# Kernel optimization log

Measured on AMD Instinct MI355X. Metric: run time of the kernel, lower is better.

The kernel has to match this reference:

```python
import jax, jax.numpy as jnp
import numpy as np

N_NODES = 50000

def _gcn_conv(x, W, b, src, dst, norm, n_nodes):
    # PyG GCNConv: linear transform, then normalized scatter-add aggregation.
    h = x @ W                                   # [N, out]
    msg = h[src] * norm[:, None]                # [E', out] gather + scale
    out = jax.ops.segment_sum(msg, dst, num_segments=n_nodes)  # scatter-add
    return out + b

def _norm_edges(edge_index, n_nodes):
    # Add self loops, compute symmetric deg^{-1/2} normalization (PyG default).
    loops = jnp.arange(n_nodes, dtype=edge_index.dtype)
    src = jnp.concatenate([edge_index[0], loops])
    dst = jnp.concatenate([edge_index[1], loops])
    deg = jax.ops.segment_sum(jnp.ones_like(dst, dtype=jnp.float32), dst,
                              num_segments=n_nodes)
    dinv = jnp.where(deg > 0, jax.lax.rsqrt(deg), 0.0)
    norm = dinv[src] * dinv[dst]
    return src, dst, norm

def setup_inputs() -> dict:
    key = jax.random.key(0)
    k1, k2, k3, k4, k5 = jax.random.split(key, 5)
    d_in, d_hid, d_out = 128, 96, 64
    x = jax.random.normal(k1, (N_NODES, d_in), dtype=jnp.float32)
    edge_index = jax.random.randint(k2, (2, 800000), 0, N_NODES, dtype=jnp.int32)
    W1 = jax.random.normal(k3, (d_in, d_hid), dtype=jnp.float32) / np.sqrt(d_in)
    b1 = jnp.zeros((d_hid,), dtype=jnp.float32)
    W2 = jax.random.normal(k4, (d_hid, d_out), dtype=jnp.float32) / np.sqrt(d_hid)
    b2 = jnp.zeros((d_out,), dtype=jnp.float32)
    return {"x": x, "edge_index": edge_index, "W1": W1, "b1": b1, "W2": W2, "b2": b2}

def reference(x, edge_index, W1, b1, W2, b2):
    n = x.shape[0]
    src, dst, norm = _norm_edges(edge_index, n)
    h = jax.nn.relu(_gcn_conv(x, W1, b1, src, dst, norm, n))
    # dropout is identity in eval mode
    out = jax.nn.relu(_gcn_conv(h, W2, b2, src, dst, norm, n))
    return out
```

## Files before the change

### kernel.cpp

```cpp
#include <hip/hip_runtime.h>

#define D_IN 128
#define D_HID 96
#define D_OUT 64
#define CHUNK 4096

template <int K, int C, int BM>
__global__ void gemm1_deg_kernel(const float* __restrict__ X, const float* __restrict__ W,
                                 float* __restrict__ H, int n, int nblkGemm,
                                 const int* __restrict__ dst, int* __restrict__ deg, int E) {
    constexpr int KT = 32;
    constexpr int TX = C / 4;
    constexpr int TY = BM / 4;
    constexpr int NTH = TX * TY;
    constexpr int WS = C + 4;
    constexpr int XS = KT + 4;
    __shared__ float Wl[KT * WS];
    __shared__ float Xl[BM * XS];

    const int tx = threadIdx.x, ty = threadIdx.y;
    const int tlin = ty * TX + tx;

    if (blockIdx.x >= nblkGemm) {
        int e0 = ((blockIdx.x - nblkGemm) * NTH + tlin) * 4;
        if (e0 + 3 < E) {
            int4 d = *(const int4*)&dst[e0];
            atomicAdd(&deg[d.x], 1);
            atomicAdd(&deg[d.y], 1);
            atomicAdd(&deg[d.z], 1);
            atomicAdd(&deg[d.w], 1);
        } else {
            for (int j = 0; j < 4; ++j) {
                int e = e0 + j;
                if (e < E) atomicAdd(&deg[dst[e]], 1);
            }
        }
        return;
    }

    const int r0 = blockIdx.x * BM;
    const int row0 = ty * 4;

    float4 acc0 = {0,0,0,0}, acc1 = {0,0,0,0}, acc2 = {0,0,0,0}, acc3 = {0,0,0,0};

    for (int kt0 = 0; kt0 < K; kt0 += KT) {
        for (int q = tlin; q < KT * (C / 4); q += NTH) {
            int k = q / (C / 4), cq = q % (C / 4);
            *(float4*)&Wl[k * WS + cq * 4] = *(const float4*)&W[(long)(kt0 + k) * C + cq * 4];
        }
        for (int q = tlin; q < BM * (KT / 4); q += NTH) {
            int r = q / (KT / 4), kq = q % (KT / 4);
            int gr = r0 + r; if (gr >= n) gr = n - 1;
            *(float4*)&Xl[r * XS + kq * 4] = *(const float4*)&X[(long)gr * K + kt0 + kq * 4];
        }
        __syncthreads();
#pragma unroll 4
        for (int k = 0; k < KT; ++k) {
            float4 w = *(const float4*)&Wl[k * WS + tx * 4];
            float x0 = Xl[(row0 + 0) * XS + k];
            float x1 = Xl[(row0 + 1) * XS + k];
            float x2 = Xl[(row0 + 2) * XS + k];
            float x3 = Xl[(row0 + 3) * XS + k];
            acc0.x = fmaf(x0, w.x, acc0.x); acc0.y = fmaf(x0, w.y, acc0.y);
            acc0.z = fmaf(x0, w.z, acc0.z); acc0.w = fmaf(x0, w.w, acc0.w);
            acc1.x = fmaf(x1, w.x, acc1.x); acc1.y = fmaf(x1, w.y, acc1.y);
            acc1.z = fmaf(x1, w.z, acc1.z); acc1.w = fmaf(x1, w.w, acc1.w);
            acc2.x = fmaf(x2, w.x, acc2.x); acc2.y = fmaf(x2, w.y, acc2.y);
            acc2.z = fmaf(x2, w.z, acc2.z); acc2.w = fmaf(x2, w.w, acc2.w);
            acc3.x = fmaf(x3, w.x, acc3.x); acc3.y = fmaf(x3, w.y, acc3.y);
            acc3.z = fmaf(x3, w.z, acc3.z); acc3.w = fmaf(x3, w.w, acc3.w);
        }
        __syncthreads();
    }

    float4 a[4] = {acc0, acc1, acc2, acc3};
#pragma unroll
    for (int i = 0; i < 4; ++i) {
        int row = r0 + row0 + i;
        if (row < n) *(float4*)&H[(long)row * C + tx * 4] = a[i];
    }
}

__global__ void scanA_kernel(const int* __restrict__ deg, int* __restrict__ partial, int n) {
    __shared__ int wsum[16];
    const int tid = threadIdx.x, lane = tid & 63, wid = tid >> 6;
    int i0 = blockIdx.x * CHUNK + tid * 4;
    int s = 0;
    if (i0 + 3 < n) {
        int4 v = *(const int4*)&deg[i0];
        s = v.x + v.y + v.z + v.w;
    } else {
        for (int j = 0; j < 4; ++j) if (i0 + j < n) s += deg[i0 + j];
    }
    for (int off = 32; off; off >>= 1) s += __shfl_down(s, off);
    if (lane == 0) wsum[wid] = s;
    __syncthreads();
    if (tid == 0) {
        int t = 0;
        for (int w = 0; w < 16; ++w) t += wsum[w];
        partial[blockIdx.x] = t;
    }
}

__global__ void scanB_kernel(const int* __restrict__ partial, int* __restrict__ offs, int nb) {
    int lane = threadIdx.x;
    int v = (lane < nb) ? partial[lane] : 0;
    int s = v;
    for (int off = 1; off < 64; off <<= 1) {
        int t = __shfl_up(s, off);
        if (lane >= off) s += t;
    }
    if (lane < nb) offs[lane] = s - v;
}

__global__ void scanC_kernel(const int* __restrict__ deg, const int* __restrict__ offs,
                             int* __restrict__ row_ptr, int* __restrict__ cursor,
                             float* __restrict__ dinv, int n) {
    __shared__ int wsum[16];
    const int tid = threadIdx.x, lane = tid & 63, wid = tid >> 6;
    const int base = offs[blockIdx.x];
    int i0 = blockIdx.x * CHUNK + tid * 4;
    int v0 = (i0 + 0 < n) ? deg[i0 + 0] : 0;
    int v1 = (i0 + 1 < n) ? deg[i0 + 1] : 0;
    int v2 = (i0 + 2 < n) ? deg[i0 + 2] : 0;
    int v3 = (i0 + 3 < n) ? deg[i0 + 3] : 0;
    int p0 = v0, p1 = p0 + v1, p2 = p1 + v2, p3 = p2 + v3;
    int tsum = p3;
    for (int off = 1; off < 64; off <<= 1) {
        int t = __shfl_up(tsum, off);
        if (lane >= off) tsum += t;
    }
    if (lane == 63) wsum[wid] = tsum;
    __syncthreads();
    if (wid == 0) {
        int w = (lane < 16) ? wsum[lane] : 0;
        for (int off = 1; off < 16; off <<= 1) {
            int t = __shfl_up(w, off);
            if (lane >= off) w += t;
        }
        if (lane < 16) wsum[lane] = w;
    }
    __syncthreads();
    int texcl = base + (wid ? wsum[wid - 1] : 0) + tsum - p3;
    int e0 = texcl, e1 = texcl + p0, e2 = texcl + p1, e3 = texcl + p2;
    if (i0 + 0 < n) { row_ptr[i0+0] = e0; cursor[i0+0] = e0; dinv[i0+0] = rsqrtf((float)v0 + 1.0f); }
    if (i0 + 1 < n) { row_ptr[i0+1] = e1; cursor[i0+1] = e1; dinv[i0+1] = rsqrtf((float)v1 + 1.0f); }
    if (i0 + 2 < n) { row_ptr[i0+2] = e2; cursor[i0+2] = e2; dinv[i0+2] = rsqrtf((float)v2 + 1.0f); }
    if (i0 + 3 < n) { row_ptr[i0+3] = e3; cursor[i0+3] = e3; dinv[i0+3] = rsqrtf((float)v3 + 1.0f); }
}

__global__ void fill_kernel(const int* __restrict__ src, const int* __restrict__ dst,
                            int* __restrict__ cursor, unsigned short* __restrict__ srcIdx, int E) {
    int e0 = (blockIdx.x * blockDim.x + threadIdx.x) * 4;
    if (e0 + 3 < E) {
        int4 d = *(const int4*)&dst[e0];
        int4 s = *(const int4*)&src[e0];
        int p0 = atomicAdd(&cursor[d.x], 1);
        int p1 = atomicAdd(&cursor[d.y], 1);
        int p2 = atomicAdd(&cursor[d.z], 1);
        int p3 = atomicAdd(&cursor[d.w], 1);
        srcIdx[p0] = (unsigned short)s.x;
        srcIdx[p1] = (unsigned short)s.y;
        srcIdx[p2] = (unsigned short)s.z;
        srcIdx[p3] = (unsigned short)s.w;
    } else {
        for (int j = 0; j < 4; ++j) {
            int e = e0 + j;
            if (e < E) {
                int pos = atomicAdd(&cursor[dst[e]], 1);
                srcIdx[pos] = (unsigned short)src[e];
            }
        }
    }
}

template <int K, int C, int BM>
__global__ void gemm_tiled_kernel(const float* __restrict__ X, const float* __restrict__ W,
                                  const float* __restrict__ dinv, float* __restrict__ H, int n) {
    constexpr int KT = 32;
    constexpr int TX = C / 4;
    constexpr int TY = BM / 4;
    constexpr int NTH = TX * TY;
    constexpr int WS = C + 4;
    constexpr int XS = KT + 4;
    __shared__ float Wl[KT * WS];
    __shared__ float Xl[BM * XS];

    const int tx = threadIdx.x, ty = threadIdx.y;
    const int tlin = ty * TX + tx;
    const int r0 = blockIdx.x * BM;
    const int row0 = ty * 4;

    float4 acc0 = {0,0,0,0}, acc1 = {0,0,0,0}, acc2 = {0,0,0,0}, acc3 = {0,0,0,0};

    for (int kt0 = 0; kt0 < K; kt0 += KT) {
        for (int q = tlin; q < KT * (C / 4); q += NTH) {
            int k = q / (C / 4), cq = q % (C / 4);
            *(float4*)&Wl[k * WS + cq * 4] = *(const float4*)&W[(long)(kt0 + k) * C + cq * 4];
        }
        for (int q = tlin; q < BM * (KT / 4); q += NTH) {
            int r = q / (KT / 4), kq = q % (KT / 4);
            int gr = r0 + r; if (gr >= n) gr = n - 1;
            *(float4*)&Xl[r * XS + kq * 4] = *(const float4*)&X[(long)gr * K + kt0 + kq * 4];
        }
        __syncthreads();
#pragma unroll 4
        for (int k = 0; k < KT; ++k) {
            float4 w = *(const float4*)&Wl[k * WS + tx * 4];
            float x0 = Xl[(row0 + 0) * XS + k];
            float x1 = Xl[(row0 + 1) * XS + k];
            float x2 = Xl[(row0 + 2) * XS + k];
            float x3 = Xl[(row0 + 3) * XS + k];
            acc0.x = fmaf(x0, w.x, acc0.x); acc0.y = fmaf(x0, w.y, acc0.y);
            acc0.z = fmaf(x0, w.z, acc0.z); acc0.w = fmaf(x0, w.w, acc0.w);
            acc1.x = fmaf(x1, w.x, acc1.x); acc1.y = fmaf(x1, w.y, acc1.y);
            acc1.z = fmaf(x1, w.z, acc1.z); acc1.w = fmaf(x1, w.w, acc1.w);
            acc2.x = fmaf(x2, w.x, acc2.x); acc2.y = fmaf(x2, w.y, acc2.y);
            acc2.z = fmaf(x2, w.z, acc2.z); acc2.w = fmaf(x2, w.w, acc2.w);
            acc3.x = fmaf(x3, w.x, acc3.x); acc3.y = fmaf(x3, w.y, acc3.y);
            acc3.z = fmaf(x3, w.z, acc3.z); acc3.w = fmaf(x3, w.w, acc3.w);
        }
        __syncthreads();
    }

    float4 a[4] = {acc0, acc1, acc2, acc3};
#pragma unroll
    for (int i = 0; i < 4; ++i) {
        int row = r0 + row0 + i;
        if (row < n) {
            float di = dinv[row];
            float4 o = {a[i].x * di, a[i].y * di, a[i].z * di, a[i].w * di};
            *(float4*)&H[(long)row * C + tx * 4] = o;
        }
    }
}

template <int C, int NY, bool SCALE_SRC>
__global__ void agg4_kernel(const int* __restrict__ row_ptr, const int* __restrict__ deg,
                            const unsigned short* __restrict__ srcIdx, const float* __restrict__ hs,
                            const float* __restrict__ dinv, const float* __restrict__ b,
                            float* __restrict__ out, int n) {
    int tx = threadIdx.x;
    int d = blockIdx.x * NY + threadIdx.y;
    if (d >= n) return;
    int start = row_ptr[d];
    int cnt   = deg[d];
    float di  = dinv[d];
    float4 acc = *(const float4*)&hs[(long)d * C + tx * 4];
    if (SCALE_SRC) { acc.x *= di; acc.y *= di; acc.z *= di; acc.w *= di; }
    int k = 0;
    for (; k + 3 < cnt; k += 4) {
        int s0 = srcIdx[start + k + 0];
        int s1 = srcIdx[start + k + 1];
        int s2 = srcIdx[start + k + 2];
        int s3 = srcIdx[start + k + 3];
        float4 v0 = *(const float4*)&hs[(long)s0 * C + tx * 4];
        float4 v1 = *(const float4*)&hs[(long)s1 * C + tx * 4];
        float4 v2 = *(const float4*)&hs[(long)s2 * C + tx * 4];
        float4 v3 = *(const float4*)&hs[(long)s3 * C + tx * 4];
        if (SCALE_SRC) {
            float n0 = dinv[s0], n1 = dinv[s1], n2 = dinv[s2], n3 = dinv[s3];
            acc.x = fmaf(v0.x, n0, acc.x); acc.y = fmaf(v0.y, n0, acc.y);
            acc.z = fmaf(v0.z, n0, acc.z); acc.w = fmaf(v0.w, n0, acc.w);
            acc.x = fmaf(v1.x, n1, acc.x); acc.y = fmaf(v1.y, n1, acc.y);
            acc.z = fmaf(v1.z, n1, acc.z); acc.w = fmaf(v1.w, n1, acc.w);
            acc.x = fmaf(v2.x, n2, acc.x); acc.y = fmaf(v2.y, n2, acc.y);
            acc.z = fmaf(v2.z, n2, acc.z); acc.w = fmaf(v2.w, n2, acc.w);
            acc.x = fmaf(v3.x, n3, acc.x); acc.y = fmaf(v3.y, n3, acc.y);
            acc.z = fmaf(v3.z, n3, acc.z); acc.w = fmaf(v3.w, n3, acc.w);
        } else {
            acc.x += v0.x + v1.x + v2.x + v3.x;
            acc.y += v0.y + v1.y + v2.y + v3.y;
            acc.z += v0.z + v1.z + v2.z + v3.z;
            acc.w += v0.w + v1.w + v2.w + v3.w;
        }
    }
    for (; k < cnt; ++k) {
        int s = srcIdx[start + k];
        float4 v = *(const float4*)&hs[(long)s * C + tx * 4];
        if (SCALE_SRC) {
            float nm = dinv[s];
            acc.x = fmaf(v.x, nm, acc.x); acc.y = fmaf(v.y, nm, acc.y);
            acc.z = fmaf(v.z, nm, acc.z); acc.w = fmaf(v.w, nm, acc.w);
        } else {
            acc.x += v.x; acc.y += v.y; acc.z += v.z; acc.w += v.w;
        }
    }
    const float4 bb = *(const float4*)&b[tx * 4];
    float4 o;
    o.x = fmaxf(fmaf(di, acc.x, bb.x), 0.f);
    o.y = fmaxf(fmaf(di, acc.y, bb.y), 0.f);
    o.z = fmaxf(fmaf(di, acc.z, bb.z), 0.f);
    o.w = fmaxf(fmaf(di, acc.w, bb.w), 0.f);
    *(float4*)&out[(long)d * C + tx * 4] = o;
}

extern "C" void kernel_launch(void* const* d_in, const int* in_sizes, int n_in,
                              void* d_out, int out_size, void* d_ws, size_t ws_size,
                              hipStream_t stream) {
    const float* x  = (const float*)d_in[0];
    const int*   ei = (const int*)d_in[1];
    const float* W1 = (const float*)d_in[2];
    const float* b1 = (const float*)d_in[3];
    const float* W2 = (const float*)d_in[4];
    const float* b2 = (const float*)d_in[5];
    float* out = (float*)d_out;

    const int n = in_sizes[0] / D_IN;
    const int E = in_sizes[1] / 2;
    const int* srcp = ei;
    const int* dstp = ei + E;

    char* ws = (char*)d_ws;
    float* dinv   = (float*)(ws);
    int*   deg    = (int*)  (ws + (256u << 10));
    int*   rowp   = (int*)  (ws + (512u << 10));
    int*   cursor = (int*)  (ws + (768u << 10));
    int*   partial= (int*)  (ws + (968u << 10));
    int*   offs   = (int*)  (ws + (996u << 10));
    unsigned short* srcIdx = (unsigned short*)(ws + (1u << 20));
    float* h1     = (float*)(ws + (5u << 20));
    float* act1   = (float*)(ws + (25u << 20));
    float* g2s    = h1;

    hipMemsetAsync(deg, 0, (size_t)n * sizeof(int), stream);

    const int nb = (n + CHUNK - 1) / CHUNK;
    const int BM = 64;
    const int nblk = (n + BM - 1) / BM;

    {
        const int degBlocks = (E / 4 + 383) / 384;
        dim3 blk(D_HID / 4, BM / 4);
        gemm1_deg_kernel<D_IN, D_HID, BM><<<nblk + degBlocks, blk, 0, stream>>>(
            x, W1, h1, n, nblk, dstp, deg, E);
    }

    scanA_kernel<<<nb, 1024, 0, stream>>>(deg, partial, n);
    scanB_kernel<<<1, 64, 0, stream>>>(partial, offs, nb);
    scanC_kernel<<<nb, 1024, 0, stream>>>(deg, offs, rowp, cursor, dinv, n);
    fill_kernel<<<(E / 4 + 255) / 256, 256, 0, stream>>>(srcp, dstp, cursor, srcIdx, E);

    {
        dim3 ablk(D_HID / 4, 8);
        agg4_kernel<D_HID, 8, true><<<(n + 7) / 8, ablk, 0, stream>>>(
            rowp, deg, srcIdx, h1, dinv, b1, act1, n);
    }

    {
        dim3 blk(D_OUT / 4, BM / 4);
        gemm_tiled_kernel<D_HID, D_OUT, BM><<<nblk, blk, 0, stream>>>(act1, W2, dinv, g2s, n);
        dim3 ablk(D_OUT / 4, 16);
        agg4_kernel<D_OUT, 16, false><<<(n + 15) / 16, ablk, 0, stream>>>(
            rowp, deg, srcIdx, g2s, dinv, b2, out, n);
    }
}
```

Measured before the change: 268.2 us.

## Store intermediate features in bf16 and unroll aggregation gather by eight

Intermediate node features (h1, act1, g2s) are now stored as bf16 instead of fp32, with fp32 accumulation in the GEMMs and aggregations. This halves the bytes moved by the gather-heavy aggregation kernels and the GEMM2 input load. The aggregation loop is also unrolled to eight neighbours to put more loads in flight. The cost is reduced precision in the intermediates, which may loosen agreement with the fp32 reference.

```diff
diff --git a/kernel.cpp b/kernel.cpp
--- a/kernel.cpp
+++ b/kernel.cpp
@@ -5,9 +5,20 @@
 #define D_OUT 64
 #define CHUNK 4096
 
+typedef unsigned short u16;
+
+__device__ __forceinline__ u16 f2bf(float f) {
+    unsigned u = __float_as_uint(f);
+    u += 0x7FFF + ((u >> 16) & 1);
+    return (u16)(u >> 16);
+}
+__device__ __forceinline__ float bf2f(u16 h) {
+    return __uint_as_float(((unsigned)h) << 16);
+}
+
 template <int K, int C, int BM>
 __global__ void gemm1_deg_kernel(const float* __restrict__ X, const float* __restrict__ W,
-                                 float* __restrict__ H, int n, int nblkGemm,
+                                 u16* __restrict__ H, int n, int nblkGemm,
                                  const int* __restrict__ dst, int* __restrict__ deg, int E) {
     constexpr int KT = 32;
     constexpr int TX = C / 4;
@@ -77,7 +88,10 @@
 #pragma unroll
     for (int i = 0; i < 4; ++i) {
         int row = r0 + row0 + i;
-        if (row < n) *(float4*)&H[(long)row * C + tx * 4] = a[i];
+        if (row < n) {
+            ushort4 o = { f2bf(a[i].x), f2bf(a[i].y), f2bf(a[i].z), f2bf(a[i].w) };
+            *(ushort4*)&H[(long)row * C + tx * 4] = o;
+        }
     }
 }
 
@@ -150,7 +164,7 @@
 }
 
 __global__ void fill_kernel(const int* __restrict__ src, const int* __restrict__ dst,
-                            int* __restrict__ cursor, unsigned short* __restrict__ srcIdx, int E) {
+                            int* __restrict__ cursor, u16* __restrict__ srcIdx, int E) {
     int e0 = (blockIdx.x * blockDim.x + threadIdx.x) * 4;
     if (e0 + 3 < E) {
         int4 d = *(const int4*)&dst[e0];
@@ -159,24 +173,24 @@
         int p1 = atomicAdd(&cursor[d.y], 1);
         int p2 = atomicAdd(&cursor[d.z], 1);
         int p3 = atomicAdd(&cursor[d.w], 1);
-        srcIdx[p0] = (unsigned short)s.x;
-        srcIdx[p1] = (unsigned short)s.y;
-        srcIdx[p2] = (unsigned short)s.z;
-        srcIdx[p3] = (unsigned short)s.w;
+        srcIdx[p0] = (u16)s.x;
+        srcIdx[p1] = (u16)s.y;
+        srcIdx[p2] = (u16)s.z;
+        srcIdx[p3] = (u16)s.w;
     } else {
         for (int j = 0; j < 4; ++j) {
             int e = e0 + j;
             if (e < E) {
                 int pos = atomicAdd(&cursor[dst[e]], 1);
-                srcIdx[pos] = (unsigned short)src[e];
+                srcIdx[pos] = (u16)src[e];
             }
         }
     }
 }
 
 template <int K, int C, int BM>
-__global__ void gemm_tiled_kernel(const float* __restrict__ X, const float* __restrict__ W,
-                                  const float* __restrict__ dinv, float* __restrict__ H, int n) {
+__global__ void gemm2_kernel(const u16* __restrict__ X, const float* __restrict__ W,
+                             const float* __restrict__ dinv, u16* __restrict__ H, int n) {
     constexpr int KT = 32;
     constexpr int TX = C / 4;
     constexpr int TY = BM / 4;
@@ -198,10 +212,15 @@
             int k = q / (C / 4), cq = q % (C / 4);
             *(float4*)&Wl[k * WS + cq * 4] = *(const float4*)&W[(long)(kt0 + k) * C + cq * 4];
         }
-        for (int q = tlin; q < BM * (KT / 4); q += NTH) {
-            int r = q / (KT / 4), kq = q % (KT / 4);
+        for (int q = tlin; q < BM * (KT / 8); q += NTH) {
+            int r = q / (KT / 8), kq = q % (KT / 8);
             int gr = r0 + r; if (gr >= n) gr = n - 1;
-            *(float4*)&Xl[r * XS + kq * 4] = *(const float4*)&X[(long)gr * K + kt0 + kq * 4];
+            uint4 v = *(const uint4*)&X[(long)gr * K + kt0 + kq * 8];
+            float* dr = &Xl[r * XS + kq * 8];
+            dr[0] = bf2f((u16)(v.x & 0xFFFF)); dr[1] = bf2f((u16)(v.x >> 16));
+            dr[2] = bf2f((u16)(v.y & 0xFFFF)); dr[3] = bf2f((u16)(v.y >> 16));
+            dr[4] = bf2f((u16)(v.z & 0xFFFF)); dr[5] = bf2f((u16)(v.z >> 16));
+            dr[6] = bf2f((u16)(v.w & 0xFFFF)); dr[7] = bf2f((u16)(v.w >> 16));
         }
         __syncthreads();
 #pragma unroll 4
@@ -229,61 +248,84 @@
         int row = r0 + row0 + i;
         if (row < n) {
             float di = dinv[row];
-            float4 o = {a[i].x * di, a[i].y * di, a[i].z * di, a[i].w * di};
-            *(float4*)&H[(long)row * C + tx * 4] = o;
-        }
-    }
-}
-
-template <int C, int NY, bool SCALE_SRC>
-__global__ void agg4_kernel(const int* __restrict__ row_ptr, const int* __restrict__ deg,
-                            const unsigned short* __restrict__ srcIdx, const float* __restrict__ hs,
+            ushort4 o = { f2bf(a[i].x * di), f2bf(a[i].y * di),
+                          f2bf(a[i].z * di), f2bf(a[i].w * di) };
+            *(ushort4*)&H[(long)row * C + tx * 4] = o;
+        }
+    }
+}
+
+template <int C, int NY, bool SCALE_SRC, bool OUT_BF16>
+__global__ void aggb_kernel(const int* __restrict__ row_ptr, const int* __restrict__ deg,
+                            const u16* __restrict__ srcIdx, const u16* __restrict__ hs,
                             const float* __restrict__ dinv, const float* __restrict__ b,
-                            float* __restrict__ out, int n) {
+                            void* __restrict__ outv, int n) {
     int tx = threadIdx.x;
     int d = blockIdx.x * NY + threadIdx.y;
     if (d >= n) return;
     int start = row_ptr[d];
     int cnt   = deg[d];
     float di  = dinv[d];
-    float4 acc = *(const float4*)&hs[(long)d * C + tx * 4];
+    ushort4 sv = *(const ushort4*)&hs[(long)d * C + tx * 4];
+    float4 acc = { bf2f(sv.x), bf2f(sv.y), bf2f(sv.z), bf2f(sv.w) };
     if (SCALE_SRC) { acc.x *= di; acc.y *= di; acc.z *= di; acc.w *= di; }
     int k = 0;
-    for (; k + 3 < cnt; k += 4) {
+    for (; k + 7 < cnt; k += 8) {
         int s0 = srcIdx[start + k + 0];
         int s1 = srcIdx[start + k + 1];
         int s2 = srcIdx[start + k + 2];
         int s3 = srcIdx[start + k + 3];
-        float4 v0 = *(const float4*)&hs[(long)s0 * C + tx * 4];
-        float4 v1 = *(const float4*)&hs[(long)s1 * C + tx * 4];
-        float4 v2 = *(const float4*)&hs[(long)s2 * C + tx * 4];
-        float4 v3 = *(const float4*)&hs[(long)s3 * C + tx * 4];
+        int s4 = srcIdx[start + k + 4];
+        int s5 = srcIdx[start + k + 5];
+        int s6 = srcIdx[start + k + 6];
+        int s7 = srcIdx[start + k + 7];
+        ushort4 v0 = *(const ushort4*)&hs[(long)s0 * C + tx * 4];
+        ushort4 v1 = *(const ushort4*)&hs[(long)s1 * C + tx * 4];
+        ushort4 v2 = *(const ushort4*)&hs[(long)s2 * C + tx * 4];
+        ushort4 v3 = *(const ushort4*)&hs[(long)s3 * C + tx * 4];
+        ushort4 v4 = *(const ushort4*)&hs[(long)s4 * C + tx * 4];
+        ushort4 v5 = *(const ushort4*)&hs[(long)s5 * C + tx * 4];
+        ushort4 v6 = *(const ushort4*)&hs[(long)s6 * C + tx * 4];
+        ushort4 v7 = *(const ushort4*)&hs[(long)s7 * C + tx * 4];
         if (SCALE_SRC) {
             float n0 = dinv[s0], n1 = dinv[s1], n2 = dinv[s2], n3 = dinv[s3];
-            acc.x = fmaf(v0.x, n0, acc.x); acc.y = fmaf(v0.y, n0, acc.y);
-            acc.z = fmaf(v0.z, n0, acc.z); acc.w = fmaf(v0.w, n0, acc.w);
-            acc.x = fmaf(v1.x, n1, acc.x); acc.y = fmaf(v1.y, n1, acc.y);
-            acc.z = fmaf(v1.z, n1, acc.z); acc.w = fmaf(v1.w, n1, acc.w);
-            acc.x = fmaf(v2.x, n2, acc.x); acc.y = fmaf(v2.y, n2, acc.y);
-            acc.z = fmaf(v2.z, n2, acc.z); acc.w = fmaf(v2.w, n2, acc.w);
-            acc.x = fmaf(v3.x, n3, acc.x); acc.y = fmaf(v3.y, n3, acc.y);
-            acc.z = fmaf(v3.z, n3, acc.z); acc.w = fmaf(v3.w, n3, acc.w);
+            float n4 = dinv[s4], n5 = dinv[s5], n6 = dinv[s6], n7 = dinv[s7];
+            acc.x = fmaf(bf2f(v0.x), n0, acc.x); acc.y = fmaf(bf2f(v0.y), n0, acc.y);
+            acc.z = fmaf(bf2f(v0.z), n0, acc.z); acc.w = fmaf(bf2f(v0.w), n0, acc.w);
+            acc.x = fmaf(bf2f(v1.x), n1, acc.x); acc.y = fmaf(bf2f(v1.y), n1, acc.y);
+            acc.z = fmaf(bf2f(v1.z), n1, acc.z); acc.w = fmaf(bf2f(v1.w), n1, acc.w);
+            acc.x = fmaf(bf2f(v2.x), n2, acc.x); acc.y = fmaf(bf2f(v2.y), n2, acc.y);
+            acc.z = fmaf(bf2f(v2.z), n2, acc.z); acc.w = fmaf(bf2f(v2.w), n2, acc.w);
+            acc.x = fmaf(bf2f(v3.x), n3, acc.x); acc.y = fmaf(bf2f(v3.y), n3, acc.y);
+            acc.z = fmaf(bf2f(v3.z), n3, acc.z); acc.w = fmaf(bf2f(v3.w), n3, acc.w);
+            acc.x = fmaf(bf2f(v4.x), n4, acc.x); acc.y = fmaf(bf2f(v4.y), n4, acc.y);
+            acc.z = fmaf(bf2f(v4.z), n4, acc.z); acc.w = fmaf(bf2f(v4.w), n4, acc.w);
+            acc.x = fmaf(bf2f(v5.x), n5, acc.x); acc.y = fmaf(bf2f(v5.y), n5, acc.y);
+            acc.z = fmaf(bf2f(v5.z), n5, acc.z); acc.w = fmaf(bf2f(v5.w), n5, acc.w);
+            acc.x = fmaf(bf2f(v6.x), n6, acc.x); acc.y = fmaf(bf2f(v6.y), n6, acc.y);
+            acc.z = fmaf(bf2f(v6.z), n6, acc.z); acc.w = fmaf(bf2f(v6.w), n6, acc.w);
+            acc.x = fmaf(bf2f(v7.x), n7, acc.x); acc.y = fmaf(bf2f(v7.y), n7, acc.y);
+            acc.z = fmaf(bf2f(v7.z), n7, acc.z); acc.w = fmaf(bf2f(v7.w), n7, acc.w);
         } else {
-            acc.x += v0.x + v1.x + v2.x + v3.x;
-            acc.y += v0.y + v1.y + v2.y + v3.y;
-            acc.z += v0.z + v1.z + v2.z + v3.z;
-            acc.w += v0.w + v1.w + v2.w + v3.w;
+            acc.x += ((bf2f(v0.x) + bf2f(v1.x)) + (bf2f(v2.x) + bf2f(v3.x)))
+                   + ((bf2f(v4.x) + bf2f(v5.x)) + (bf2f(v6.x) + bf2f(v7.x)));
+            acc.y += ((bf2f(v0.y) + bf2f(v1.y)) + (bf2f(v2.y) + bf2f(v3.y)))
+                   + ((bf2f(v4.y) + bf2f(v5.y)) + (bf2f(v6.y) + bf2f(v7.y)));
+            acc.z += ((bf2f(v0.z) + bf2f(v1.z)) + (bf2f(v2.z) + bf2f(v3.z)))
+                   + ((bf2f(v4.z) + bf2f(v5.z)) + (bf2f(v6.z) + bf2f(v7.z)));
+            acc.w += ((bf2f(v0.w) + bf2f(v1.w)) + (bf2f(v2.w) + bf2f(v3.w)))
+                   + ((bf2f(v4.w) + bf2f(v5.w)) + (bf2f(v6.w) + bf2f(v7.w)));
         }
     }
     for (; k < cnt; ++k) {
         int s = srcIdx[start + k];
-        float4 v = *(const float4*)&hs[(long)s * C + tx * 4];
+        ushort4 v = *(const ushort4*)&hs[(long)s * C + tx * 4];
         if (SCALE_SRC) {
             float nm = dinv[s];
-            acc.x = fmaf(v.x, nm, acc.x); acc.y = fmaf(v.y, nm, acc.y);
-            acc.z = fmaf(v.z, nm, acc.z); acc.w = fmaf(v.w, nm, acc.w);
+            acc.x = fmaf(bf2f(v.x), nm, acc.x); acc.y = fmaf(bf2f(v.y), nm, acc.y);
+            acc.z = fmaf(bf2f(v.z), nm, acc.z); acc.w = fmaf(bf2f(v.w), nm, acc.w);
         } else {
-            acc.x += v.x; acc.y += v.y; acc.z += v.z; acc.w += v.w;
+            acc.x += bf2f(v.x); acc.y += bf2f(v.y); acc.z += bf2f(v.z); acc.w += bf2f(v.w);
         }
     }
     const float4 bb = *(const float4*)&b[tx * 4];
@@ -292,7 +334,12 @@
     o.y = fmaxf(fmaf(di, acc.y, bb.y), 0.f);
     o.z = fmaxf(fmaf(di, acc.z, bb.z), 0.f);
     o.w = fmaxf(fmaf(di, acc.w, bb.w), 0.f);
-    *(float4*)&out[(long)d * C + tx * 4] = o;
+    if (OUT_BF16) {
+        ushort4 ov = { f2bf(o.x), f2bf(o.y), f2bf(o.z), f2bf(o.w) };
+        *(ushort4*)&((u16*)outv)[(long)d * C + tx * 4] = ov;
+    } else {
+        *(float4*)&((float*)outv)[(long)d * C + tx * 4] = o;
+    }
 }
 
 extern "C" void kernel_launch(void* const* d_in, const int* in_sizes, int n_in,
@@ -318,10 +365,10 @@
     int*   cursor = (int*)  (ws + (768u << 10));
     int*   partial= (int*)  (ws + (968u << 10));
     int*   offs   = (int*)  (ws + (996u << 10));
-    unsigned short* srcIdx = (unsigned short*)(ws + (1u << 20));
-    float* h1     = (float*)(ws + (5u << 20));
-    float* act1   = (float*)(ws + (25u << 20));
-    float* g2s    = h1;
+    u16*   srcIdx = (u16*)  (ws + (1u << 20));
+    u16*   h1     = (u16*)  (ws + (5u << 20));
+    u16*   act1   = (u16*)  (ws + (16u << 20));
+    u16*   g2s    = h1;
 
     hipMemsetAsync(deg, 0, (size_t)n * sizeof(int), stream);
 
@@ -343,15 +390,15 @@
 
     {
         dim3 ablk(D_HID / 4, 8);
-        agg4_kernel<D_HID, 8, true><<<(n + 7) / 8, ablk, 0, stream>>>(
+        aggb_kernel<D_HID, 8, true, true><<<(n + 7) / 8, ablk, 0, stream>>>(
             rowp, deg, srcIdx, h1, dinv, b1, act1, n);
     }
 
     {
         dim3 blk(D_OUT / 4, BM / 4);
-        gemm_tiled_kernel<D_HID, D_OUT, BM><<<nblk, blk, 0, stream>>>(act1, W2, dinv, g2s, n);
+        gemm2_kernel<D_HID, D_OUT, BM><<<nblk, blk, 0, stream>>>(act1, W2, dinv, g2s, n);
         dim3 ablk(D_OUT / 4, 16);
-        agg4_kernel<D_OUT, 16, false><<<(n + 15) / 16, ablk, 0, stream>>>(
+        aggb_kernel<D_OUT, 16, false, false><<<(n + 15) / 16, ablk, 0, stream>>>(
             rowp, deg, srcIdx, g2s, dinv, b2, out, n);
     }
 }
```

After: 258.5 us. 1.04x faster.
